# Optimization experiments

Measured on AMD Instinct MI355X. Metric: run time of the kernel, lower is better.

The kernel has to match this reference:

```python
import jax, jax.numpy as jnp
import numpy as np

DIM = 1024
NUM_HEADS = 16
HEAD_DIM = DIM // NUM_HEADS
SCALE = HEAD_DIM ** -0.5


def setup_inputs() -> dict:
    key = jax.random.key(0)
    k1, k2, k3, k4 = jax.random.split(key, 4)
    B, N = 2, 2048
    x = jax.random.normal(k1, (B, N, DIM), dtype=jnp.float32)
    # qkv: Linear(dim, 3*dim, bias=False); torch stores weight as [out, in]
    W_qkv = jax.random.normal(k2, (3 * DIM, DIM), dtype=jnp.float32) * (DIM ** -0.5)
    # proj: Linear(dim, dim, bias=True)
    W_proj = jax.random.normal(k3, (DIM, DIM), dtype=jnp.float32) * (DIM ** -0.5)
    b_proj = jax.random.normal(k4, (DIM,), dtype=jnp.float32) * 0.01
    return {"x": x, "W_qkv": W_qkv, "W_proj": W_proj, "b_proj": b_proj}


def reference(x, W_qkv, W_proj, b_proj):
    B, N, C = x.shape
    H, D = NUM_HEADS, HEAD_DIM
    # qkv projection: [B,N,3C] -> [3,B,H,N,D]
    qkv = jnp.einsum('bnc,oc->bno', x, W_qkv)
    qkv = qkv.reshape(B, N, 3, H, D).transpose(2, 0, 3, 1, 4)
    q, k, v = qkv[0] * SCALE, qkv[1], qkv[2]
    # full attention matrix [B,H,N,N] (faithful to manual impl)
    attn = jnp.einsum('bhqd,bhkd->bhqk', q, k)
    attn = jax.nn.softmax(attn, axis=-1)
    # dropout p=0.0 -> identity (eval semantics)
    out = jnp.einsum('bhqk,bhkd->bhqd', attn, v)  # [B,H,N,D]
    out = out.transpose(0, 2, 1, 3).reshape(B, N, C)
    out = jnp.einsum('bnc,oc->bno', out, W_proj) + b_proj
    return out
```

## Files before the change

### kernel.cpp

```cpp
#include <hip/hip_runtime.h>
#include <math.h>

#define BATCH 2
#define NTOK  2048
#define DIMC  1024
#define NH    16
#define HD    64
#define SOFT_K2 0.18033688011112042f

typedef __bf16 bf16;
typedef __attribute__((ext_vector_type(8))) __bf16 bf16x8;
typedef __attribute__((ext_vector_type(4))) __bf16 bf16x4;
typedef __attribute__((ext_vector_type(4))) float f32x4;

__device__ __forceinline__ void load_lds16(const void* g, void* l) {
    __builtin_amdgcn_global_load_lds(
        (const __attribute__((address_space(1))) void*)g,
        (__attribute__((address_space(3))) void*)l, 16, 0, 0);
}
__device__ __forceinline__ f32x4 mfma16(bf16x8 a, bf16x8 b, f32x4 c) {
    return __builtin_amdgcn_mfma_f32_16x16x32_bf16(a, b, c, 0, 0, 0);
}

__global__ __launch_bounds__(256) void cast3(
    const float* __restrict__ x,  const float* __restrict__ w1, const float* __restrict__ w2,
    bf16* __restrict__ xb, bf16* __restrict__ w1b, bf16* __restrict__ w2b)
{
    int blk = blockIdx.x;
    const float* src; bf16* dst; size_t base;
    if (blk < 4096)      { src = x;  dst = xb;  base = (size_t)blk * 1024; }
    else if (blk < 7168) { src = w1; dst = w1b; base = (size_t)(blk - 4096) * 1024; }
    else                 { src = w2; dst = w2b; base = (size_t)(blk - 7168) * 1024; }
    size_t i = base + (size_t)threadIdx.x * 4;
    float4 v = *(const float4*)(src + i);
    bf16x4 r;
    r[0] = (bf16)v.x; r[1] = (bf16)v.y; r[2] = (bf16)v.z; r[3] = (bf16)v.w;
    *(bf16x4*)(dst + i) = r;
}

template<int BM, int BN, bool OUT_BF16>
__global__ __launch_bounds__(256) void gemm_bt(
    const bf16* __restrict__ A, const bf16* __restrict__ B,
    const float* __restrict__ bias, void* __restrict__ Cout,
    int M, int N, int K)
{
    __shared__ __align__(16) bf16 As[BM * 32];
    __shared__ __align__(16) bf16 Bs[BN * 32];

    constexpr int WM = BM / 2, WN = BN / 2;
    constexpr int TA = BM / 64, TB = BN / 64;

    const int tid  = threadIdx.x;
    const int w    = tid >> 6, lane = tid & 63;
    const int wm   = w & 1,  wn = w >> 1;
    const int m0   = blockIdx.y * BM, n0 = blockIdx.x * BN;
    const int lm   = lane & 15, quad = lane >> 4;

    const bf16* Ag[TA]; const bf16* Bg[TB];
#pragma unroll
    for (int t = 0; t < TA; ++t) {
        int c = t * 256 + tid;
        Ag[t] = A + (size_t)(m0 + (c % BM)) * K + (c / BM) * 8;
    }
#pragma unroll
    for (int t = 0; t < TB; ++t) {
        int c = t * 256 + tid;
        Bg[t] = B + (size_t)(n0 + (c % BN)) * K + (c / BN) * 8;
    }

    f32x4 acc[WM / 16][WN / 16];
    f32x4 z4 = {0.f, 0.f, 0.f, 0.f};
#pragma unroll
    for (int i = 0; i < WM / 16; ++i)
#pragma unroll
        for (int j = 0; j < WN / 16; ++j) acc[i][j] = z4;

    for (int kt = 0; kt < K; kt += 32) {
        __syncthreads();
#pragma unroll
        for (int t = 0; t < TA; ++t)
            load_lds16(Ag[t] + kt, As + (t * 256 + w * 64) * 8);
#pragma unroll
        for (int t = 0; t < TB; ++t)
            load_lds16(Bg[t] + kt, Bs + (t * 256 + w * 64) * 8);
        __syncthreads();

        bf16x8 af[WM / 16], bf_[WN / 16];
#pragma unroll
        for (int mi = 0; mi < WM / 16; ++mi)
            af[mi] = *(const bf16x8*)(As + (quad * BM + wm * WM + mi * 16 + lm) * 8);
#pragma unroll
        for (int ni = 0; ni < WN / 16; ++ni)
            bf_[ni] = *(const bf16x8*)(Bs + (quad * BN + wn * WN + ni * 16 + lm) * 8);
#pragma unroll
        for (int mi = 0; mi < WM / 16; ++mi)
#pragma unroll
            for (int ni = 0; ni < WN / 16; ++ni)
                acc[mi][ni] = mfma16(af[mi], bf_[ni], acc[mi][ni]);
    }

#pragma unroll
    for (int ni = 0; ni < WN / 16; ++ni) {
        const int col = n0 + wn * WN + ni * 16 + lm;
        const float bi = (!OUT_BF16 && bias) ? bias[col] : 0.0f;
#pragma unroll
        for (int mi = 0; mi < WM / 16; ++mi)
#pragma unroll
            for (int r = 0; r < 4; ++r) {
                const int row = m0 + wm * WM + mi * 16 + quad * 4 + r;
                const float v = acc[mi][ni][r] + bi;
                if (OUT_BF16) ((bf16*)Cout)[(size_t)row * N + col] = (bf16)v;
                else          ((float*)Cout)[(size_t)row * N + col] = v;
            }
    }
}

__global__ __launch_bounds__(256) void transpose_v(
    const bf16* __restrict__ qkv, bf16* __restrict__ Vt)
{
    __shared__ bf16 T[64][72];
    const int n0 = blockIdx.x * 64, h = blockIdx.y, b = blockIdx.z;
    const int tid = threadIdx.x;
    const int a = tid >> 2;
    const int c = tid & 3;
#pragma unroll
    for (int it = 0; it < 4; ++it) {
        int d0 = (c + it * 4) * 4;
        bf16x4 v = *(const bf16x4*)(qkv + (size_t)(b * NTOK + n0 + a) * (3 * DIMC)
                                    + 2 * DIMC + h * HD + d0);
        T[d0 + 0][a] = v[0]; T[d0 + 1][a] = v[1];
        T[d0 + 2][a] = v[2]; T[d0 + 3][a] = v[3];
    }
    __syncthreads();
#pragma unroll
    for (int it = 0; it < 4; ++it) {
        int n1 = (c + it * 4) * 4;
        bf16x4 o;
        o[0] = T[a][n1]; o[1] = T[a][n1 + 1]; o[2] = T[a][n1 + 2]; o[3] = T[a][n1 + 3];
        *(bf16x4*)(Vt + ((size_t)((b * NH + h) * HD + a)) * NTOK + n0 + n1) = o;
    }
}

__global__ __launch_bounds__(256, 2) void attn_mfma(
    const bf16* __restrict__ qkv,
    const bf16* __restrict__ Vt,
    bf16* __restrict__ att)
{
    __shared__ __align__(16) bf16 Qs[128 * 64];
    __shared__ __align__(16) bf16 Ks[2][64 * 64];
    __shared__ __align__(16) bf16 Vs[2][64 * 64];
    __shared__ __align__(16) bf16 Ps[128 * 72];

    const int n0 = blockIdx.x * 128, h = blockIdx.y, b = blockIdx.z;
    const int tid = threadIdx.x, w = tid >> 6, lane = tid & 63;
    const int lm = lane & 15, quad = lane >> 4;

    const size_t rs = (size_t)(3 * DIMC);
    const bf16* qbase  = qkv + (size_t)b * NTOK * rs + h * HD;
    const bf16* kbase  = qbase + DIMC;
    const bf16* vtbase = Vt + ((size_t)(b * NH + h) * HD) * NTOK;

#pragma unroll
    for (int t = 0; t < 4; ++t) {
        const int l = t * 256 + tid;
        load_lds16(qbase + (size_t)(n0 + (l & 127)) * rs + (l >> 7) * 8,
                   Qs + (t * 256 + w * 64) * 8);
    }

    const int l0 = (w * 2 + 0) * 64 + lane, l1 = (w * 2 + 1) * 64 + lane;
    const bf16* kg0 = kbase + (size_t)(l0 & 63) * rs + (l0 >> 6) * 8;
    const bf16* kg1 = kbase + (size_t)(l1 & 63) * rs + (l1 >> 6) * 8;
    const bf16* vg0 = vtbase + (size_t)(l0 & 63) * NTOK + (l0 >> 6) * 8;
    const bf16* vg1 = vtbase + (size_t)(l1 & 63) * NTOK + (l1 >> 6) * 8;

    load_lds16(kg0, Ks[0] + (w * 2 + 0) * 512);
    load_lds16(kg1, Ks[0] + (w * 2 + 1) * 512);
    load_lds16(vg0, Vs[0] + (w * 2 + 0) * 512);
    load_lds16(vg1, Vs[0] + (w * 2 + 1) * 512);

    f32x4 O[2][4];
    f32x4 z4 = {0.f, 0.f, 0.f, 0.f};
#pragma unroll
    for (int g = 0; g < 2; ++g)
#pragma unroll
        for (int ni = 0; ni < 4; ++ni) O[g][ni] = z4;
    float lsum[2][4] = {{0.f, 0.f, 0.f, 0.f}, {0.f, 0.f, 0.f, 0.f}};

    const int NT = NTOK / 64;
    for (int t = 0; t < NT; ++t) {
        const int buf = t & 1;
        __syncthreads();
        if (t + 1 < NT) {
            const size_t koff = (size_t)(t + 1) * 64 * rs;
            const size_t voff = (size_t)(t + 1) * 64;
            load_lds16(kg0 + koff, Ks[buf ^ 1] + (w * 2 + 0) * 512);
            load_lds16(kg1 + koff, Ks[buf ^ 1] + (w * 2 + 1) * 512);
            load_lds16(vg0 + voff, Vs[buf ^ 1] + (w * 2 + 0) * 512);
            load_lds16(vg1 + voff, Vs[buf ^ 1] + (w * 2 + 1) * 512);
        }

        f32x4 S[2][4];
#pragma unroll
        for (int g = 0; g < 2; ++g)
#pragma unroll
            for (int ni = 0; ni < 4; ++ni) S[g][ni] = z4;
#pragma unroll
        for (int s2 = 0; s2 < 2; ++s2) {
            bf16x8 aq0 = *(const bf16x8*)(Qs + ((s2 * 4 + quad) * 128 + w * 32 + lm) * 8);
            bf16x8 aq1 = *(const bf16x8*)(Qs + ((s2 * 4 + quad) * 128 + w * 32 + 16 + lm) * 8);
#pragma unroll
            for (int ni = 0; ni < 4; ++ni) {
                bf16x8 bk = *(const bf16x8*)(Ks[buf] + ((s2 * 4 + quad) * 64 + ni * 16 + lm) * 8);
                S[0][ni] = mfma16(aq0, bk, S[0][ni]);
                S[1][ni] = mfma16(aq1, bk, S[1][ni]);
            }
        }

#pragma unroll
        for (int g = 0; g < 2; ++g)
#pragma unroll
            for (int ni = 0; ni < 4; ++ni)
#pragma unroll
                for (int r = 0; r < 4; ++r) {
                    const float p = __builtin_amdgcn_exp2f(S[g][ni][r] * SOFT_K2);
                    Ps[(w * 32 + g * 16 + quad * 4 + r) * 72 + ni * 16 + lm] = (bf16)p;
                    lsum[g][r] += p;
                }

#pragma unroll
        for (int s2 = 0; s2 < 2; ++s2) {
            bf16x8 ap0 = *(const bf16x8*)(Ps + (w * 32 + lm) * 72 + s2 * 32 + quad * 8);
            bf16x8 ap1 = *(const bf16x8*)(Ps + (w * 32 + 16 + lm) * 72 + s2 * 32 + quad * 8);
#pragma unroll
            for (int ni = 0; ni < 4; ++ni) {
                bf16x8 bv = *(const bf16x8*)(Vs[buf] + ((s2 * 4 + quad) * 64 + ni * 16 + lm) * 8);
                O[0][ni] = mfma16(ap0, bv, O[0][ni]);
                O[1][ni] = mfma16(ap1, bv, O[1][ni]);
            }
        }
    }

#pragma unroll
    for (int g = 0; g < 2; ++g)
#pragma unroll
        for (int r = 0; r < 4; ++r) {
#pragma unroll
            for (int msk = 1; msk < 16; msk <<= 1)
                lsum[g][r] += __shfl_xor(lsum[g][r], msk);
        }

#pragma unroll
    for (int g = 0; g < 2; ++g)
#pragma unroll
        for (int r = 0; r < 4; ++r) {
            const float invl = 1.0f / lsum[g][r];
            const size_t row = (size_t)(b * NTOK + n0 + w * 32 + g * 16 + quad * 4 + r);
#pragma unroll
            for (int ni = 0; ni < 4; ++ni)
                att[row * DIMC + h * HD + ni * 16 + lm] = (bf16)(O[g][ni][r] * invl);
        }
}

extern "C" void kernel_launch(void* const* d_in, const int* in_sizes, int n_in,
                              void* d_out, int out_size, void* d_ws, size_t ws_size,
                              hipStream_t stream)
{
    const float* x      = (const float*)d_in[0];
    const float* W_qkv  = (const float*)d_in[1];
    const float* W_proj = (const float*)d_in[2];
    const float* b_proj = (const float*)d_in[3];
    float* out = (float*)d_out;

    char* ws = (char*)d_ws;
    bf16* xb   = (bf16*)ws;
    bf16* w1b  = (bf16*)(ws + (8u  << 20));
    bf16* w2b  = (bf16*)(ws + (14u << 20));
    bf16* qkvb = (bf16*)(ws + (16u << 20));
    bf16* vt   = (bf16*)(ws + (40u << 20));
    bf16* attb = (bf16*)(ws + (48u << 20));

    const int M = BATCH * NTOK;

    cast3<<<8192, 256, 0, stream>>>(x, W_qkv, W_proj, xb, w1b, w2b);

    gemm_bt<128, 128, true><<<dim3((3 * DIMC) / 128, M / 128), 256, 0, stream>>>(
        xb, w1b, nullptr, qkvb, M, 3 * DIMC, DIMC);

    transpose_v<<<dim3(NTOK / 64, NH, BATCH), 256, 0, stream>>>(qkvb, vt);

    attn_mfma<<<dim3(NTOK / 128, NH, BATCH), 256, 0, stream>>>(qkvb, vt, attb);

    gemm_bt<64, 128, false><<<dim3(DIMC / 128, M / 64), 256, 0, stream>>>(
        attb, w2b, b_proj, out, M, DIMC, DIMC);
}
```

Measured before the change: 230.7 us.

## Fuse V transpose into QKV GEMM epilogue and software-pipeline attention S/PV stages

The QKV GEMM epilogue now writes the V columns directly in transposed [B,H,D,N] layout, which removes the separate transpose_v kernel launch and its extra read and write of V. The attention kernel keeps Q fragments in registers instead of LDS and double-buffers the P tile. This lets QK^T plus exp for tile t+1 run while PV for tile t is issued, with K prefetched two tiles ahead. The cost is more LDS for P, more registers, and strided 8-byte stores in the V epilogue.

```diff
diff --git a/kernel.cpp b/kernel.cpp
--- a/kernel.cpp
+++ b/kernel.cpp
@@ -38,106 +38,153 @@
     *(bf16x4*)(dst + i) = r;
 }
 
-template<int BM, int BN, bool OUT_BF16>
-__global__ __launch_bounds__(256) void gemm_bt(
+__global__ __launch_bounds__(256) void gemm_qkv(
     const bf16* __restrict__ A, const bf16* __restrict__ B,
-    const float* __restrict__ bias, void* __restrict__ Cout,
+    bf16* __restrict__ Cq, bf16* __restrict__ vt,
     int M, int N, int K)
 {
-    __shared__ __align__(16) bf16 As[BM * 32];
-    __shared__ __align__(16) bf16 Bs[BN * 32];
-
-    constexpr int WM = BM / 2, WN = BN / 2;
-    constexpr int TA = BM / 64, TB = BN / 64;
+    __shared__ __align__(16) bf16 As[128 * 32];
+    __shared__ __align__(16) bf16 Bs[128 * 32];
 
     const int tid  = threadIdx.x;
     const int w    = tid >> 6, lane = tid & 63;
     const int wm   = w & 1,  wn = w >> 1;
-    const int m0   = blockIdx.y * BM, n0 = blockIdx.x * BN;
+    const int m0   = blockIdx.y * 128, n0 = blockIdx.x * 128;
     const int lm   = lane & 15, quad = lane >> 4;
 
-    const bf16* Ag[TA]; const bf16* Bg[TB];
-#pragma unroll
-    for (int t = 0; t < TA; ++t) {
+    const bf16* Ag[2]; const bf16* Bg[2];
+#pragma unroll
+    for (int t = 0; t < 2; ++t) {
         int c = t * 256 + tid;
-        Ag[t] = A + (size_t)(m0 + (c % BM)) * K + (c / BM) * 8;
-    }
-#pragma unroll
-    for (int t = 0; t < TB; ++t) {
+        Ag[t] = A + (size_t)(m0 + (c & 127)) * K + (c >> 7) * 8;
+        Bg[t] = B + (size_t)(n0 + (c & 127)) * K + (c >> 7) * 8;
+    }
+
+    f32x4 acc[4][4];
+    f32x4 z4 = {0.f, 0.f, 0.f, 0.f};
+#pragma unroll
+    for (int i = 0; i < 4; ++i)
+#pragma unroll
+        for (int j = 0; j < 4; ++j) acc[i][j] = z4;
+
+    for (int kt = 0; kt < K; kt += 32) {
+        __syncthreads();
+#pragma unroll
+        for (int t = 0; t < 2; ++t) {
+            load_lds16(Ag[t] + kt, As + (t * 256 + w * 64) * 8);
+            load_lds16(Bg[t] + kt, Bs + (t * 256 + w * 64) * 8);
+        }
+        __syncthreads();
+
+        bf16x8 af[4], bf_[4];
+#pragma unroll
+        for (int mi = 0; mi < 4; ++mi)
+            af[mi] = *(const bf16x8*)(As + (quad * 128 + wm * 64 + mi * 16 + lm) * 8);
+#pragma unroll
+        for (int ni = 0; ni < 4; ++ni)
+            bf_[ni] = *(const bf16x8*)(Bs + (quad * 128 + wn * 64 + ni * 16 + lm) * 8);
+#pragma unroll
+        for (int mi = 0; mi < 4; ++mi)
+#pragma unroll
+            for (int ni = 0; ni < 4; ++ni)
+                acc[mi][ni] = mfma16(af[mi], bf_[ni], acc[mi][ni]);
+    }
+
+    if (n0 >= 2048) {
+#pragma unroll
+        for (int ni = 0; ni < 4; ++ni) {
+            const int c  = n0 + wn * 64 + ni * 16 + lm - 2048;
+            const int hh = c >> 6, dd = c & 63;
+#pragma unroll
+            for (int mi = 0; mi < 4; ++mi) {
+                const int rowb = m0 + wm * 64 + mi * 16 + quad * 4;
+                const int bb = rowb >> 11, tok = rowb & 2047;
+                bf16x4 pk;
+                pk[0] = (bf16)acc[mi][ni][0]; pk[1] = (bf16)acc[mi][ni][1];
+                pk[2] = (bf16)acc[mi][ni][2]; pk[3] = (bf16)acc[mi][ni][3];
+                *(bf16x4*)(vt + ((size_t)((bb * NH + hh) * HD + dd)) * NTOK + tok) = pk;
+            }
+        }
+    } else {
+#pragma unroll
+        for (int ni = 0; ni < 4; ++ni) {
+            const int col = n0 + wn * 64 + ni * 16 + lm;
+#pragma unroll
+            for (int mi = 0; mi < 4; ++mi)
+#pragma unroll
+                for (int r = 0; r < 4; ++r) {
+                    const int row = m0 + wm * 64 + mi * 16 + quad * 4 + r;
+                    Cq[(size_t)row * N + col] = (bf16)acc[mi][ni][r];
+                }
+        }
+    }
+}
+
+__global__ __launch_bounds__(256) void gemm_proj(
+    const bf16* __restrict__ A, const bf16* __restrict__ B,
+    const float* __restrict__ bias, float* __restrict__ C,
+    int M, int N, int K)
+{
+    __shared__ __align__(16) bf16 As[64 * 32];
+    __shared__ __align__(16) bf16 Bs[128 * 32];
+
+    const int tid  = threadIdx.x;
+    const int w    = tid >> 6, lane = tid & 63;
+    const int wm   = w & 1,  wn = w >> 1;
+    const int m0   = blockIdx.y * 64, n0 = blockIdx.x * 128;
+    const int lm   = lane & 15, quad = lane >> 4;
+
+    const bf16* Ag; const bf16* Bg[2];
+    {
+        int c = tid;
+        Ag = A + (size_t)(m0 + (c & 63)) * K + (c >> 6) * 8;
+    }
+#pragma unroll
+    for (int t = 0; t < 2; ++t) {
         int c = t * 256 + tid;
-        Bg[t] = B + (size_t)(n0 + (c % BN)) * K + (c / BN) * 8;
-    }
-
-    f32x4 acc[WM / 16][WN / 16];
+        Bg[t] = B + (size_t)(n0 + (c & 127)) * K + (c >> 7) * 8;
+    }
+
+    f32x4 acc[2][4];
     f32x4 z4 = {0.f, 0.f, 0.f, 0.f};
 #pragma unroll
-    for (int i = 0; i < WM / 16; ++i)
-#pragma unroll
-        for (int j = 0; j < WN / 16; ++j) acc[i][j] = z4;
+    for (int i = 0; i < 2; ++i)
+#pragma unroll
+        for (int j = 0; j < 4; ++j) acc[i][j] = z4;
 
     for (int kt = 0; kt < K; kt += 32) {
         __syncthreads();
-#pragma unroll
-        for (int t = 0; t < TA; ++t)
-            load_lds16(Ag[t] + kt, As + (t * 256 + w * 64) * 8);
-#pragma unroll
-        for (int t = 0; t < TB; ++t)
+        load_lds16(Ag + kt, As + (w * 64) * 8);
+#pragma unroll
+        for (int t = 0; t < 2; ++t)
             load_lds16(Bg[t] + kt, Bs + (t * 256 + w * 64) * 8);
         __syncthreads();
 
-        bf16x8 af[WM / 16], bf_[WN / 16];
-#pragma unroll
-        for (int mi = 0; mi < WM / 16; ++mi)
-            af[mi] = *(const bf16x8*)(As + (quad * BM + wm * WM + mi * 16 + lm) * 8);
-#pragma unroll
-        for (int ni = 0; ni < WN / 16; ++ni)
-            bf_[ni] = *(const bf16x8*)(Bs + (quad * BN + wn * WN + ni * 16 + lm) * 8);
-#pragma unroll
-        for (int mi = 0; mi < WM / 16; ++mi)
-#pragma unroll
-            for (int ni = 0; ni < WN / 16; ++ni)
+        bf16x8 af[2], bf_[4];
+#pragma unroll
+        for (int mi = 0; mi < 2; ++mi)
+            af[mi] = *(const bf16x8*)(As + (quad * 64 + wm * 32 + mi * 16 + lm) * 8);
+#pragma unroll
+        for (int ni = 0; ni < 4; ++ni)
+            bf_[ni] = *(const bf16x8*)(Bs + (quad * 128 + wn * 64 + ni * 16 + lm) * 8);
+#pragma unroll
+        for (int mi = 0; mi < 2; ++mi)
+#pragma unroll
+            for (int ni = 0; ni < 4; ++ni)
                 acc[mi][ni] = mfma16(af[mi], bf_[ni], acc[mi][ni]);
     }
 
 #pragma unroll
-    for (int ni = 0; ni < WN / 16; ++ni) {
-        const int col = n0 + wn * WN + ni * 16 + lm;
-        const float bi = (!OUT_BF16 && bias) ? bias[col] : 0.0f;
-#pragma unroll
-        for (int mi = 0; mi < WM / 16; ++mi)
+    for (int ni = 0; ni < 4; ++ni) {
+        const int col = n0 + wn * 64 + ni * 16 + lm;
+        const float bi = bias[col];
+#pragma unroll
+        for (int mi = 0; mi < 2; ++mi)
 #pragma unroll
             for (int r = 0; r < 4; ++r) {
-                const int row = m0 + wm * WM + mi * 16 + quad * 4 + r;
-                const float v = acc[mi][ni][r] + bi;
-                if (OUT_BF16) ((bf16*)Cout)[(size_t)row * N + col] = (bf16)v;
-                else          ((float*)Cout)[(size_t)row * N + col] = v;
+                const int row = m0 + wm * 32 + mi * 16 + quad * 4 + r;
+                C[(size_t)row * N + col] = acc[mi][ni][r] + bi;
             }
-    }
-}
-
-__global__ __launch_bounds__(256) void transpose_v(
-    const bf16* __restrict__ qkv, bf16* __restrict__ Vt)
-{
-    __shared__ bf16 T[64][72];
-    const int n0 = blockIdx.x * 64, h = blockIdx.y, b = blockIdx.z;
-    const int tid = threadIdx.x;
-    const int a = tid >> 2;
-    const int c = tid & 3;
-#pragma unroll
-    for (int it = 0; it < 4; ++it) {
-        int d0 = (c + it * 4) * 4;
-        bf16x4 v = *(const bf16x4*)(qkv + (size_t)(b * NTOK + n0 + a) * (3 * DIMC)
-                                    + 2 * DIMC + h * HD + d0);
-        T[d0 + 0][a] = v[0]; T[d0 + 1][a] = v[1];
-        T[d0 + 2][a] = v[2]; T[d0 + 3][a] = v[3];
-    }
-    __syncthreads();
-#pragma unroll
-    for (int it = 0; it < 4; ++it) {
-        int n1 = (c + it * 4) * 4;
-        bf16x4 o;
-        o[0] = T[a][n1]; o[1] = T[a][n1 + 1]; o[2] = T[a][n1 + 2]; o[3] = T[a][n1 + 3];
-        *(bf16x4*)(Vt + ((size_t)((b * NH + h) * HD + a)) * NTOK + n0 + n1) = o;
     }
 }
 
@@ -146,10 +193,9 @@
     const bf16* __restrict__ Vt,
     bf16* __restrict__ att)
 {
-    __shared__ __align__(16) bf16 Qs[128 * 64];
     __shared__ __align__(16) bf16 Ks[2][64 * 64];
     __shared__ __align__(16) bf16 Vs[2][64 * 64];
-    __shared__ __align__(16) bf16 Ps[128 * 72];
+    __shared__ __align__(16) bf16 Ps[2][128 * 72];
 
     const int n0 = blockIdx.x * 128, h = blockIdx.y, b = blockIdx.z;
     const int tid = threadIdx.x, w = tid >> 6, lane = tid & 63;
@@ -160,12 +206,13 @@
     const bf16* kbase  = qbase + DIMC;
     const bf16* vtbase = Vt + ((size_t)(b * NH + h) * HD) * NTOK;
 
-#pragma unroll
-    for (int t = 0; t < 4; ++t) {
-        const int l = t * 256 + tid;
-        load_lds16(qbase + (size_t)(n0 + (l & 127)) * rs + (l >> 7) * 8,
-                   Qs + (t * 256 + w * 64) * 8);
-    }
+    bf16x8 aq[2][2];
+#pragma unroll
+    for (int g = 0; g < 2; ++g)
+#pragma unroll
+        for (int s2 = 0; s2 < 2; ++s2)
+            aq[g][s2] = *(const bf16x8*)(qbase
+                + (size_t)(n0 + w * 32 + g * 16 + lm) * rs + s2 * 32 + quad * 8);
 
     const int l0 = (w * 2 + 0) * 64 + lane, l1 = (w * 2 + 1) * 64 + lane;
     const bf16* kg0 = kbase + (size_t)(l0 & 63) * rs + (l0 >> 6) * 8;
@@ -173,10 +220,12 @@
     const bf16* vg0 = vtbase + (size_t)(l0 & 63) * NTOK + (l0 >> 6) * 8;
     const bf16* vg1 = vtbase + (size_t)(l1 & 63) * NTOK + (l1 >> 6) * 8;
 
-    load_lds16(kg0, Ks[0] + (w * 2 + 0) * 512);
-    load_lds16(kg1, Ks[0] + (w * 2 + 1) * 512);
-    load_lds16(vg0, Vs[0] + (w * 2 + 0) * 512);
-    load_lds16(vg1, Vs[0] + (w * 2 + 1) * 512);
+#define STAGE_K(tile, dst) do { \
+    load_lds16(kg0 + (size_t)(tile) * 64 * rs, (dst) + (w * 2 + 0) * 512); \
+    load_lds16(kg1 + (size_t)(tile) * 64 * rs, (dst) + (w * 2 + 1) * 512); } while (0)
+#define STAGE_V(tile, dst) do { \
+    load_lds16(vg0 + (size_t)(tile) * 64, (dst) + (w * 2 + 0) * 512); \
+    load_lds16(vg1 + (size_t)(tile) * 64, (dst) + (w * 2 + 1) * 512); } while (0)
 
     f32x4 O[2][4];
     f32x4 z4 = {0.f, 0.f, 0.f, 0.f};
@@ -186,59 +235,62 @@
         for (int ni = 0; ni < 4; ++ni) O[g][ni] = z4;
     float lsum[2][4] = {{0.f, 0.f, 0.f, 0.f}, {0.f, 0.f, 0.f, 0.f}};
 
+#define COMPUTE_S_PS(Ksb, Psb) do {                                           \
+    f32x4 S[2][4];                                                            \
+    for (int g = 0; g < 2; ++g)                                               \
+        for (int ni = 0; ni < 4; ++ni) S[g][ni] = z4;                         \
+    for (int s2 = 0; s2 < 2; ++s2)                                            \
+        for (int ni = 0; ni < 4; ++ni) {                                      \
+            bf16x8 bk = *(const bf16x8*)((Ksb)                                \
+                + ((s2 * 4 + quad) * 64 + ni * 16 + lm) * 8);                 \
+            S[0][ni] = mfma16(aq[0][s2], bk, S[0][ni]);                       \
+            S[1][ni] = mfma16(aq[1][s2], bk, S[1][ni]);                       \
+        }                                                                     \
+    for (int g = 0; g < 2; ++g)                                               \
+        for (int ni = 0; ni < 4; ++ni)                                        \
+            for (int r = 0; r < 4; ++r) {                                     \
+                const float p = __builtin_amdgcn_exp2f(S[g][ni][r] * SOFT_K2);\
+                (Psb)[(w * 32 + g * 16 + quad * 4 + r) * 72 + ni * 16 + lm]   \
+                    = (bf16)p;                                                \
+                lsum[g][r] += p;                                              \
+            }                                                                 \
+} while (0)
+
+#define COMPUTE_PV(Psb, Vsb) do {                                             \
+    for (int s2 = 0; s2 < 2; ++s2) {                                          \
+        bf16x8 ap0 = *(const bf16x8*)((Psb)                                   \
+            + (w * 32 + lm) * 72 + s2 * 32 + quad * 8);                       \
+        bf16x8 ap1 = *(const bf16x8*)((Psb)                                   \
+            + (w * 32 + 16 + lm) * 72 + s2 * 32 + quad * 8);                  \
+        for (int ni = 0; ni < 4; ++ni) {                                      \
+            bf16x8 bv = *(const bf16x8*)((Vsb)                                \
+                + ((s2 * 4 + quad) * 64 + ni * 16 + lm) * 8);                 \
+            O[0][ni] = mfma16(ap0, bv, O[0][ni]);                             \
+            O[1][ni] = mfma16(ap1, bv, O[1][ni]);                             \
+        }                                                                     \
+    }                                                                         \
+} while (0)
+
     const int NT = NTOK / 64;
+
+    STAGE_K(0, Ks[0]);
+    STAGE_V(0, Vs[0]);
+    STAGE_K(1, Ks[1]);
+    __syncthreads();
+    COMPUTE_S_PS(Ks[0], Ps[0]);
+
     for (int t = 0; t < NT; ++t) {
-        const int buf = t & 1;
-        __syncthreads();
-        if (t + 1 < NT) {
-            const size_t koff = (size_t)(t + 1) * 64 * rs;
-            const size_t voff = (size_t)(t + 1) * 64;
-            load_lds16(kg0 + koff, Ks[buf ^ 1] + (w * 2 + 0) * 512);
-            load_lds16(kg1 + koff, Ks[buf ^ 1] + (w * 2 + 1) * 512);
-            load_lds16(vg0 + voff, Vs[buf ^ 1] + (w * 2 + 0) * 512);
-            load_lds16(vg1 + voff, Vs[buf ^ 1] + (w * 2 + 1) * 512);
-        }
-
-        f32x4 S[2][4];
-#pragma unroll
-        for (int g = 0; g < 2; ++g)
-#pragma unroll
-            for (int ni = 0; ni < 4; ++ni) S[g][ni] = z4;
-#pragma unroll
-        for (int s2 = 0; s2 < 2; ++s2) {
-            bf16x8 aq0 = *(const bf16x8*)(Qs + ((s2 * 4 + quad) * 128 + w * 32 + lm) * 8);
-            bf16x8 aq1 = *(const bf16x8*)(Qs + ((s2 * 4 + quad) * 128 + w * 32 + 16 + lm) * 8);
-#pragma unroll
-            for (int ni = 0; ni < 4; ++ni) {
-                bf16x8 bk = *(const bf16x8*)(Ks[buf] + ((s2 * 4 + quad) * 64 + ni * 16 + lm) * 8);
-                S[0][ni] = mfma16(aq0, bk, S[0][ni]);
-                S[1][ni] = mfma16(aq1, bk, S[1][ni]);
-            }
-        }
-
-#pragma unroll
-        for (int g = 0; g < 2; ++g)
-#pragma unroll
-            for (int ni = 0; ni < 4; ++ni)
-#pragma unroll
-                for (int r = 0; r < 4; ++r) {
-                    const float p = __builtin_amdgcn_exp2f(S[g][ni][r] * SOFT_K2);
-                    Ps[(w * 32 + g * 16 + quad * 4 + r) * 72 + ni * 16 + lm] = (bf16)p;
-                    lsum[g][r] += p;
-                }
-
-#pragma unroll
-        for (int s2 = 0; s2 < 2; ++s2) {
-            bf16x8 ap0 = *(const bf16x8*)(Ps + (w * 32 + lm) * 72 + s2 * 32 + quad * 8);
-            bf16x8 ap1 = *(const bf16x8*)(Ps + (w * 32 + 16 + lm) * 72 + s2 * 32 + quad * 8);
-#pragma unroll
-            for (int ni = 0; ni < 4; ++ni) {
-                bf16x8 bv = *(const bf16x8*)(Vs[buf] + ((s2 * 4 + quad) * 64 + ni * 16 + lm) * 8);
-                O[0][ni] = mfma16(ap0, bv, O[0][ni]);
-                O[1][ni] = mfma16(ap1, bv, O[1][ni]);
-            }
-        }
-    }
+        __syncthreads();
+        if (t + 2 < NT) STAGE_K(t + 2, Ks[t & 1]);
+        if (t + 1 < NT) STAGE_V(t + 1, Vs[(t + 1) & 1]);
+        if (t + 1 < NT) COMPUTE_S_PS(Ks[(t + 1) & 1], Ps[(t + 1) & 1]);
+        COMPUTE_PV(Ps[t & 1], Vs[t & 1]);
+    }
+
+#undef STAGE_K
+#undef STAGE_V
+#undef COMPUTE_S_PS
+#undef COMPUTE_PV
 
 #pragma unroll
     for (int g = 0; g < 2; ++g)
@@ -283,13 +335,11 @@
 
     cast3<<<8192, 256, 0, stream>>>(x, W_qkv, W_proj, xb, w1b, w2b);
 
-    gemm_bt<128, 128, true><<<dim3((3 * DIMC) / 128, M / 128), 256, 0, stream>>>(
-        xb, w1b, nullptr, qkvb, M, 3 * DIMC, DIMC);
-
-    transpose_v<<<dim3(NTOK / 64, NH, BATCH), 256, 0, stream>>>(qkvb, vt);
+    gemm_qkv<<<dim3((3 * DIMC) / 128, M / 128), 256, 0, stream>>>(
+        xb, w1b, qkvb, vt, M, 3 * DIMC, DIMC);
 
     attn_mfma<<<dim3(NTOK / 128, NH, BATCH), 256, 0, stream>>>(qkvb, vt, attb);
 
-    gemm_bt<64, 128, false><<<dim3(DIMC / 128, M / 64), 256, 0, stream>>>(
+    gemm_proj<<<dim3(DIMC / 128, M / 64), 256, 0, stream>>>(
         attb, w2b, b_proj, out, M, DIMC, DIMC);
 }
```

After: 232.8 us. No clear change (+0.9%).
